# Kernel optimization log

Hardware: AMD Instinct MI355X
Metric: run time of the kernel (lower is better)

The kernel has to match this reference:

```python
import jax, jax.numpy as jnp
import numpy as np


def setup_inputs() -> dict:
    key = jax.random.key(0)
    ks = jax.random.split(key, 8)
    B, N, D, E = 8, 64, 64, 32
    nodes = jax.random.normal(ks[0], (B, N, D), dtype=jnp.float32)
    edges = jax.random.normal(ks[1], (B, N * N, E), dtype=jnp.float32)
    mask = jax.random.uniform(ks[2], (B, N * N, 1), dtype=jnp.float32)
    W_e = jax.random.normal(ks[3], (E, D * D), dtype=jnp.float32) * 0.05
    b_e = jnp.zeros((D * D,), dtype=jnp.float32)
    gru_kernel = jax.random.normal(ks[4], (D, 3 * D), dtype=jnp.float32) * 0.05
    gru_rkernel = jax.random.normal(ks[5], (D, 3 * D), dtype=jnp.float32) * 0.05
    gru_bias = jnp.zeros((2, 3 * D), dtype=jnp.float32)
    return {"nodes": nodes, "edges": edges, "mask": mask, "W_e": W_e,
            "b_e": b_e, "gru_kernel": gru_kernel, "gru_rkernel": gru_rkernel,
            "gru_bias": gru_bias}


def _gru_step(x, h, K, R, bias):
    # keras GRU with reset_after=True
    D = h.shape[-1]
    xk = x @ K + bias[0]          # [M, 3D]
    hk = h @ R + bias[1]          # [M, 3D]
    xz, xr, xh = xk[:, :D], xk[:, D:2 * D], xk[:, 2 * D:]
    hz, hr, hh_ = hk[:, :D], hk[:, D:2 * D], hk[:, 2 * D:]
    z = jax.nn.sigmoid(xz + hz)
    r = jax.nn.sigmoid(xr + hr)
    hh = jnp.tanh(xh + r * hh_)
    return z * h + (1.0 - z) * hh


def reference(nodes, edges, mask, W_e, b_e, gru_kernel, gru_rkernel, gru_bias):
    B, N, D = nodes.shape
    # edge-conditioned transform matrices: [B, N*N, D, D]
    A = jax.nn.relu(edges @ W_e + b_e).reshape(B, N * N, D, D)
    # state_j = tile(nodes, [1, N, 1]) -> [B, N*N, D]
    state_j = jnp.tile(nodes, (1, N, 1))
    # per-edge small matmul A @ node_j
    messages = jnp.einsum('beij,bej->bei', A, state_j)  # [B, N*N, D]
    masked = (messages * mask).reshape(B, N, N, D)
    agg = masked.sum(axis=2)  # [B, N, D]
    # GRU over length-2 sequence [old_state, agg_messages], batch B*N, h0=0
    h = jnp.zeros((B * N, D), dtype=nodes.dtype)
    h = _gru_step(nodes.reshape(B * N, D), h, gru_kernel, gru_rkernel, gru_bias)
    h = _gru_step(agg.reshape(B * N, D), h, gru_kernel, gru_rkernel, gru_bias)
    return h.reshape(B, N, D)
```

## Files before the change

### kernel.cpp

```cpp
#include <hip/hip_runtime.h>

typedef _Float16 half8 __attribute__((ext_vector_type(8)));
typedef float floatx4 __attribute__((ext_vector_type(4)));
typedef float floatx2 __attribute__((ext_vector_type(2)));
typedef unsigned int uintx2 __attribute__((ext_vector_type(2)));

#define BB 8
#define NN 64
#define DD 64
#define EE 32

__device__ __forceinline__ float sigmoidf_(float x) { return 1.f / (1.f + __expf(-x)); }
__device__ __forceinline__ float tanhf_(float x) {
    float e = __expf(2.f * x);
    return (e - 1.f) / (e + 1.f);
}
__device__ __forceinline__ floatx2 relu2(floatx2 v) {
    floatx2 z = {0.f, 0.f};
    return __builtin_elementwise_max(v, z);
}

__global__ void prep_kernel(const float* __restrict__ W_e, _Float16* __restrict__ WT) {
    const int tid = threadIdx.x;
    const int d   = blockIdx.x * 64 + (tid & 63);
    const int kq  = tid >> 6;
    half8 buf;
#pragma unroll
    for (int j = 0; j < 8; ++j)
        buf[j] = (_Float16)W_e[(kq * 8 + j) * 4096 + d];
    *reinterpret_cast<half8*>(WT + d * 32 + kq * 8) = buf;
}

__global__ __launch_bounds__(512, 4)
void fused_kernel(const _Float16* __restrict__ WT,
                  const float* __restrict__ edges,
                  const float* __restrict__ nodes,
                  const float* __restrict__ mask,
                  const float* __restrict__ b_e,
                  const float* __restrict__ K,
                  const float* __restrict__ R,
                  const float* __restrict__ bias,
                  float* __restrict__ out) {
    const int b     = blockIdx.x >> 6;
    const int inode = blockIdx.x & 63;
    const int tid   = threadIdx.x;
    const int w     = tid >> 6;
    const int jw    = w & 3;
    const int ibase = (w >> 2) * 32;
    const int lane  = tid & 63;
    const int quad  = lane >> 4;
    const int col   = lane & 15;
    const int row   = b * 64 + inode;

    __shared__ float S[4][32][65];
    __shared__ float P[4][64];
    __shared__ float aggs[64], h1s[64], ns[64];
    __shared__ float gx[192], g1[192], g2[192];

    if (tid < 64) ns[tid] = nodes[row * 64 + tid];

    half8 ef[4];
#pragma unroll
    for (int eb = 0; eb < 4; ++eb) {
        const float* ep = edges + (b * 4096 + inode * 64 + eb * 16 + col) * 32 + quad * 8;
        floatx4 e0 = *reinterpret_cast<const floatx4*>(ep);
        floatx4 e1 = *reinterpret_cast<const floatx4*>(ep + 4);
#pragma unroll
        for (int j = 0; j < 4; ++j) {
            ef[eb][j]     = (_Float16)e0[j];
            ef[eb][4 + j] = (_Float16)e1[j];
        }
    }

    floatx2 xm[4][2];
#pragma unroll
    for (int eb = 0; eb < 4; ++eb) {
        int j = eb * 16 + col;
        float mk = mask[b * 4096 + inode * 64 + j];
#pragma unroll
        for (int r = 0; r < 4; ++r) {
            int jj = jw * 16 + quad * 4 + r;
            xm[eb][r >> 1][r & 1] = mk * nodes[(b * 64 + j) * 64 + jj];
        }
    }

    const _Float16* aptr = WT + (jw * 16 + col) * 32 + quad * 8;
    const float*    bptr = b_e + jw * 16 + quad * 4;

    half8   af0 = *reinterpret_cast<const half8*>(aptr + ibase * 2048);
    floatx4 bf0 = *reinterpret_cast<const floatx4*>(bptr + ibase * 64);
    half8   af1 = *reinterpret_cast<const half8*>(aptr + (ibase + 1) * 2048);
    floatx4 bf1 = *reinterpret_cast<const floatx4*>(bptr + (ibase + 1) * 64);

    for (int ii = 0; ii < 32; ++ii) {
        int ip2 = ibase + ((ii + 2) & 31);
        half8   afn = *reinterpret_cast<const half8*>(aptr + ip2 * 2048);
        floatx4 bfn = *reinterpret_cast<const floatx4*>(bptr + ip2 * 64);

        floatx4 c[4];
        c[0] = __builtin_amdgcn_mfma_f32_16x16x32_f16(af0, ef[0], bf0, 0, 0, 0);
        c[1] = __builtin_amdgcn_mfma_f32_16x16x32_f16(af0, ef[1], bf0, 0, 0, 0);
        c[2] = __builtin_amdgcn_mfma_f32_16x16x32_f16(af0, ef[2], bf0, 0, 0, 0);
        c[3] = __builtin_amdgcn_mfma_f32_16x16x32_f16(af0, ef[3], bf0, 0, 0, 0);

        floatx2 sv = {0.f, 0.f};
#pragma unroll
        for (int eb = 0; eb < 4; ++eb) {
            floatx2* cp = reinterpret_cast<floatx2*>(&c[eb]);
            sv += relu2(cp[0]) * xm[eb][0];
            sv += relu2(cp[1]) * xm[eb][1];
        }
        float s = sv[0] + sv[1];

#if __has_builtin(__builtin_amdgcn_permlane32_swap)
        uintx2 pr = __builtin_amdgcn_permlane32_swap(__float_as_uint(s), __float_as_uint(s),
                                                     false, false);
        s = __uint_as_float(pr[0]) + __uint_as_float(pr[1]);
#else
        s += __shfl_xor(s, 32);
#endif
        if (lane < 32) S[jw][lane][ibase + ii] = s;

        af0 = af1; bf0 = bf1; af1 = afn; bf1 = bfn;
    }
    __syncthreads();

    if (tid < 256) {
        int ii = tid & 63, ww = tid >> 6;
        float p = 0.f;
#pragma unroll
        for (int l = 0; l < 32; ++l) p += S[ww][l][ii];
        P[ww][ii] = p;
    } else if (tid < 448) {
        int t = tid - 256;
        float a = bias[t];
#pragma unroll 8
        for (int k = 0; k < 64; ++k) a = fmaf(ns[k], K[k * 192 + t], a);
        gx[t] = a;
    }
    __syncthreads();

    if (tid < 64) {
        aggs[tid] = P[0][tid] + P[1][tid] + P[2][tid] + P[3][tid];
    } else if (tid < 128) {
        int d = tid - 64;
        float z  = sigmoidf_(gx[d]       + bias[192 + d]);
        float r  = sigmoidf_(gx[64 + d]  + bias[256 + d]);
        float hh = tanhf_   (gx[128 + d] + r * bias[320 + d]);
        h1s[d] = (1.f - z) * hh;
    }
    __syncthreads();

    if (tid < 192) {
        float a1 = bias[tid];
#pragma unroll 8
        for (int k = 0; k < 64; ++k) a1 = fmaf(aggs[k], K[k * 192 + tid], a1);
        g1[tid] = a1;
    } else if (tid < 384) {
        int t = tid - 192;
        float a2 = bias[192 + t];
#pragma unroll 8
        for (int k = 0; k < 64; ++k) a2 = fmaf(h1s[k], R[k * 192 + t], a2);
        g2[t] = a2;
    }
    __syncthreads();

    if (tid < 64) {
        float z  = sigmoidf_(g1[tid]       + g2[tid]);
        float r  = sigmoidf_(g1[64 + tid]  + g2[64 + tid]);
        float hh = tanhf_   (g1[128 + tid] + r * g2[128 + tid]);
        out[row * 64 + tid] = z * h1s[tid] + (1.f - z) * hh;
    }
}

extern "C" void kernel_launch(void* const* d_in, const int* in_sizes, int n_in,
                              void* d_out, int out_size, void* d_ws, size_t ws_size,
                              hipStream_t stream) {
    const float* nodes = (const float*)d_in[0];
    const float* edges = (const float*)d_in[1];
    const float* mask  = (const float*)d_in[2];
    const float* W_e   = (const float*)d_in[3];
    const float* b_e   = (const float*)d_in[4];
    const float* gk    = (const float*)d_in[5];
    const float* gr    = (const float*)d_in[6];
    const float* gb    = (const float*)d_in[7];
    float* out = (float*)d_out;

    _Float16* WT = (_Float16*)d_ws;

    prep_kernel<<<64, 256, 0, stream>>>(W_e, WT);
    fused_kernel<<<512, 512, 0, stream>>>(WT, edges, nodes, mask, b_e, gk, gr, gb, out);
}
```

Measured before the change: 94.86 us.

## Process two destination nodes per block and read W_e directly, dropping prep kernel

```diff
diff --git a/kernel.cpp b/kernel.cpp
--- a/kernel.cpp
+++ b/kernel.cpp
@@ -20,19 +20,8 @@
     return __builtin_elementwise_max(v, z);
 }
 
-__global__ void prep_kernel(const float* __restrict__ W_e, _Float16* __restrict__ WT) {
-    const int tid = threadIdx.x;
-    const int d   = blockIdx.x * 64 + (tid & 63);
-    const int kq  = tid >> 6;
-    half8 buf;
-#pragma unroll
-    for (int j = 0; j < 8; ++j)
-        buf[j] = (_Float16)W_e[(kq * 8 + j) * 4096 + d];
-    *reinterpret_cast<half8*>(WT + d * 32 + kq * 8) = buf;
-}
-
-__global__ __launch_bounds__(512, 4)
-void fused_kernel(const _Float16* __restrict__ WT,
+__global__ __launch_bounds__(512, 2)
+void fused_kernel(const float* __restrict__ W_e,
                   const float* __restrict__ edges,
                   const float* __restrict__ nodes,
                   const float* __restrict__ mask,
@@ -41,28 +30,32 @@
                   const float* __restrict__ R,
                   const float* __restrict__ bias,
                   float* __restrict__ out) {
-    const int b     = blockIdx.x >> 6;
-    const int inode = blockIdx.x & 63;
-    const int tid   = threadIdx.x;
-    const int w     = tid >> 6;
-    const int jw    = w & 3;
-    const int ibase = (w >> 2) * 32;
-    const int lane  = tid & 63;
-    const int quad  = lane >> 4;
-    const int col   = lane & 15;
-    const int row   = b * 64 + inode;
-
-    __shared__ float S[4][32][65];
-    __shared__ float P[4][64];
-    __shared__ float aggs[64], h1s[64], ns[64];
-    __shared__ float gx[192], g1[192], g2[192];
-
-    if (tid < 64) ns[tid] = nodes[row * 64 + tid];
-
-    half8 ef[4];
-#pragma unroll
-    for (int eb = 0; eb < 4; ++eb) {
-        const float* ep = edges + (b * 4096 + inode * 64 + eb * 16 + col) * 32 + quad * 8;
+    const int b      = blockIdx.x >> 5;
+    const int pairi  = blockIdx.x & 31;
+    const int inode0 = pairi * 2;
+    const int tid    = threadIdx.x;
+    const int w      = tid >> 6;
+    const int jw     = w & 3;
+    const int ibase  = (w >> 2) * 32;
+    const int lane   = tid & 63;
+    const int quad   = lane >> 4;
+    const int col    = lane & 15;
+
+    __shared__ float S[2][4][16][65];
+    __shared__ float P[2][4][64];
+    __shared__ float aggs[2][64], h1s[2][64], ns[2][64];
+    __shared__ float gx[2][192], g1[2][192], g2[2][192];
+
+    if (tid < 128) {
+        int g = tid >> 6, d = tid & 63;
+        ns[g][d] = nodes[(b * 64 + inode0 + g) * 64 + d];
+    }
+
+    half8 ef[8];
+    const float* ebase = edges + (size_t)(b * 4096 + inode0 * 64) * 32;
+#pragma unroll
+    for (int eb = 0; eb < 8; ++eb) {
+        const float* ep = ebase + (eb * 16 + col) * 32 + quad * 8;
         floatx4 e0 = *reinterpret_cast<const floatx4*>(ep);
         floatx4 e1 = *reinterpret_cast<const floatx4*>(ep + 4);
 #pragma unroll
@@ -72,104 +65,142 @@
         }
     }
 
-    floatx2 xm[4][2];
-#pragma unroll
-    for (int eb = 0; eb < 4; ++eb) {
-        int j = eb * 16 + col;
-        float mk = mask[b * 4096 + inode * 64 + j];
-#pragma unroll
-        for (int r = 0; r < 4; ++r) {
-            int jj = jw * 16 + quad * 4 + r;
-            xm[eb][r >> 1][r & 1] = mk * nodes[(b * 64 + j) * 64 + jj];
+    floatx2 nd[4][2];
+#pragma unroll
+    for (int q4 = 0; q4 < 4; ++q4) {
+        int j = q4 * 16 + col;
+#pragma unroll
+        for (int rp = 0; rp < 2; ++rp) {
+            int jj = jw * 16 + quad * 4 + rp * 2;
+            nd[q4][rp][0] = nodes[(b * 64 + j) * 64 + jj];
+            nd[q4][rp][1] = nodes[(b * 64 + j) * 64 + jj + 1];
         }
     }
-
-    const _Float16* aptr = WT + (jw * 16 + col) * 32 + quad * 8;
-    const float*    bptr = b_e + jw * 16 + quad * 4;
-
-    half8   af0 = *reinterpret_cast<const half8*>(aptr + ibase * 2048);
+    floatx2 xm[8][2];
+#pragma unroll
+    for (int eb = 0; eb < 8; ++eb) {
+        float mk = mask[b * 4096 + inode0 * 64 + eb * 16 + col];
+        xm[eb][0] = nd[eb & 3][0] * mk;
+        xm[eb][1] = nd[eb & 3][1] * mk;
+    }
+
+    const float* wb   = W_e + (size_t)(quad * 8) * 4096 + jw * 16 + col;
+    const float* bptr = b_e + jw * 16 + quad * 4;
+
+    float fA[8];
+    auto LDW = [&](int i) {
+#pragma unroll
+        for (int j = 0; j < 8; ++j) fA[j] = wb[(size_t)j * 4096 + i * 64];
+    };
+    auto CVT = [&]() {
+        half8 a;
+#pragma unroll
+        for (int j = 0; j < 8; ++j) a[j] = (_Float16)fA[j];
+        return a;
+    };
+
+    LDW(ibase);
     floatx4 bf0 = *reinterpret_cast<const floatx4*>(bptr + ibase * 64);
-    half8   af1 = *reinterpret_cast<const half8*>(aptr + (ibase + 1) * 2048);
     floatx4 bf1 = *reinterpret_cast<const floatx4*>(bptr + (ibase + 1) * 64);
+    half8 af0 = CVT();
+    LDW(ibase + 1);
+    half8 af1 = CVT();
 
     for (int ii = 0; ii < 32; ++ii) {
         int ip2 = ibase + ((ii + 2) & 31);
-        half8   afn = *reinterpret_cast<const half8*>(aptr + ip2 * 2048);
+        LDW(ip2);
         floatx4 bfn = *reinterpret_cast<const floatx4*>(bptr + ip2 * 64);
 
-        floatx4 c[4];
-        c[0] = __builtin_amdgcn_mfma_f32_16x16x32_f16(af0, ef[0], bf0, 0, 0, 0);
-        c[1] = __builtin_amdgcn_mfma_f32_16x16x32_f16(af0, ef[1], bf0, 0, 0, 0);
-        c[2] = __builtin_amdgcn_mfma_f32_16x16x32_f16(af0, ef[2], bf0, 0, 0, 0);
-        c[3] = __builtin_amdgcn_mfma_f32_16x16x32_f16(af0, ef[3], bf0, 0, 0, 0);
-
-        floatx2 sv = {0.f, 0.f};
-#pragma unroll
-        for (int eb = 0; eb < 4; ++eb) {
-            floatx2* cp = reinterpret_cast<floatx2*>(&c[eb]);
-            sv += relu2(cp[0]) * xm[eb][0];
-            sv += relu2(cp[1]) * xm[eb][1];
+        floatx4 c[8];
+#pragma unroll
+        for (int eb = 0; eb < 8; ++eb)
+            c[eb] = __builtin_amdgcn_mfma_f32_16x16x32_f16(af0, ef[eb], bf0, 0, 0, 0);
+
+#pragma unroll
+        for (int g = 0; g < 2; ++g) {
+            floatx2 sv = {0.f, 0.f};
+#pragma unroll
+            for (int e4 = 0; e4 < 4; ++e4) {
+                int eb = g * 4 + e4;
+                floatx2* cp = reinterpret_cast<floatx2*>(&c[eb]);
+                sv += relu2(cp[0]) * xm[eb][0];
+                sv += relu2(cp[1]) * xm[eb][1];
+            }
+            float s = sv[0] + sv[1];
+            uintx2 p32 = __builtin_amdgcn_permlane32_swap(__float_as_uint(s), __float_as_uint(s),
+                                                          false, false);
+            s = __uint_as_float(p32[0]) + __uint_as_float(p32[1]);
+#if __has_builtin(__builtin_amdgcn_permlane16_swap)
+            uintx2 p16 = __builtin_amdgcn_permlane16_swap(__float_as_uint(s), __float_as_uint(s),
+                                                          false, false);
+            s = __uint_as_float(p16[0]) + __uint_as_float(p16[1]);
+#else
+            s += __shfl_xor(s, 16);
+#endif
+            if (lane < 16) S[g][jw][lane][ibase + ii] = s;
         }
-        float s = sv[0] + sv[1];
-
-#if __has_builtin(__builtin_amdgcn_permlane32_swap)
-        uintx2 pr = __builtin_amdgcn_permlane32_swap(__float_as_uint(s), __float_as_uint(s),
-                                                     false, false);
-        s = __uint_as_float(pr[0]) + __uint_as_float(pr[1]);
-#else
-        s += __shfl_xor(s, 32);
-#endif
-        if (lane < 32) S[jw][lane][ibase + ii] = s;
-
+
+        half8 afn = CVT();
         af0 = af1; bf0 = bf1; af1 = afn; bf1 = bfn;
     }
     __syncthreads();
 
-    if (tid < 256) {
-        int ii = tid & 63, ww = tid >> 6;
+    {
+        int g = tid >> 8, ww = (tid >> 6) & 3, ii = tid & 63;
         float p = 0.f;
 #pragma unroll
-        for (int l = 0; l < 32; ++l) p += S[ww][l][ii];
-        P[ww][ii] = p;
-    } else if (tid < 448) {
-        int t = tid - 256;
+        for (int l = 0; l < 16; ++l) p += S[g][ww][l][ii];
+        P[g][ww][ii] = p;
+    }
+    __syncthreads();
+
+    if (tid < 128) {
+        int g = tid >> 6, d = tid & 63;
+        aggs[g][d] = P[g][0][d] + P[g][1][d] + P[g][2][d] + P[g][3][d];
+    } else {
+        int u = tid - 128;
+        int g = (u >= 192) ? 1 : 0;
+        int t = u - g * 192;
         float a = bias[t];
 #pragma unroll 8
-        for (int k = 0; k < 64; ++k) a = fmaf(ns[k], K[k * 192 + t], a);
-        gx[t] = a;
-    }
-    __syncthreads();
-
-    if (tid < 64) {
-        aggs[tid] = P[0][tid] + P[1][tid] + P[2][tid] + P[3][tid];
-    } else if (tid < 128) {
-        int d = tid - 64;
-        float z  = sigmoidf_(gx[d]       + bias[192 + d]);
-        float r  = sigmoidf_(gx[64 + d]  + bias[256 + d]);
-        float hh = tanhf_   (gx[128 + d] + r * bias[320 + d]);
-        h1s[d] = (1.f - z) * hh;
-    }
-    __syncthreads();
-
-    if (tid < 192) {
-        float a1 = bias[tid];
+        for (int k = 0; k < 64; ++k) a = fmaf(ns[g][k], K[k * 192 + t], a);
+        gx[g][t] = a;
+    }
+    __syncthreads();
+
+    if (tid < 128) {
+        int g = tid >> 6, d = tid & 63;
+        float z  = sigmoidf_(gx[g][d]        + bias[192 + d]);
+        float r  = sigmoidf_(gx[g][64 + d]   + bias[256 + d]);
+        float hh = tanhf_   (gx[g][128 + d]  + r * bias[320 + d]);
+        h1s[g][d] = (1.f - z) * hh;
+    } else {
+        int u = tid - 128;
+        int g = (u >= 192) ? 1 : 0;
+        int t = u - g * 192;
+        float a = bias[t];
 #pragma unroll 8
-        for (int k = 0; k < 64; ++k) a1 = fmaf(aggs[k], K[k * 192 + tid], a1);
-        g1[tid] = a1;
-    } else if (tid < 384) {
-        int t = tid - 192;
-        float a2 = bias[192 + t];
+        for (int k = 0; k < 64; ++k) a = fmaf(aggs[g][k], K[k * 192 + t], a);
+        g1[g][t] = a;
+    }
+    __syncthreads();
+
+    if (tid < 384) {
+        int g = (tid >= 192) ? 1 : 0;
+        int t = tid - g * 192;
+        float a = bias[192 + t];
 #pragma unroll 8
-        for (int k = 0; k < 64; ++k) a2 = fmaf(h1s[k], R[k * 192 + t], a2);
-        g2[t] = a2;
-    }
-    __syncthreads();
-
-    if (tid < 64) {
-        float z  = sigmoidf_(g1[tid]       + g2[tid]);
-        float r  = sigmoidf_(g1[64 + tid]  + g2[64 + tid]);
-        float hh = tanhf_   (g1[128 + tid] + r * g2[128 + tid]);
-        out[row * 64 + tid] = z * h1s[tid] + (1.f - z) * hh;
+        for (int k = 0; k < 64; ++k) a = fmaf(h1s[g][k], R[k * 192 + t], a);
+        g2[g][t] = a;
+    }
+    __syncthreads();
+
+    if (tid < 128) {
+        int g = tid >> 6, d = tid & 63;
+        float z  = sigmoidf_(g1[g][d]       + g2[g][d]);
+        float r  = sigmoidf_(g1[g][64 + d]  + g2[g][64 + d]);
+        float hh = tanhf_   (g1[g][128 + d] + r * g2[g][128 + d]);
+        out[(b * 64 + inode0 + g) * 64 + d] = z * h1s[g][d] + (1.f - z) * hh;
     }
 }
 
@@ -186,8 +217,7 @@
     const float* gb    = (const float*)d_in[7];
     float* out = (float*)d_out;
 
-    _Float16* WT = (_Float16*)d_ws;
-
-    prep_kernel<<<64, 256, 0, stream>>>(W_e, WT);
-    fused_kernel<<<512, 512, 0, stream>>>(WT, edges, nodes, mask, b_e, gk, gr, gb, out);
-}
+    (void)d_ws; (void)ws_size;
+
+    fused_kernel<<<256, 512, 0, stream>>>(W_e, edges, nodes, mask, b_e, gk, gr, gb, out);
+}
```

Measured after the change: 102.2 us. 1.08x slower.
